# Kernel tuning notes

Hardware: AMD Instinct MI355X
Metric: run time of the kernel (lower is better)

The kernel has to match this reference:

```python
import jax, jax.numpy as jnp
import numpy as np

N, B, D = 100000, 1024, 768  # total nodes, num graphs, feature dim
DE = 64                      # placeholder edge-feat dim (unused, passed through)


def setup_inputs() -> dict:
    key = jax.random.key(0)
    ks = jax.random.split(key, 6)
    feat = jax.random.normal(ks[0], (N, D), jnp.float32)
    vn_feat = jax.random.normal(ks[1], (B, D), jnp.float32)
    edge_feat = jax.random.normal(ks[2], (B, DE), jnp.float32)
    batch = jnp.sort(jax.random.randint(ks[3], (N,), 0, B)).astype(jnp.int32)
    fc_W = jax.random.normal(ks[4], (D, D), jnp.float32) * 0.02
    fc_b = jnp.zeros((D,), jnp.float32)
    proj_W = jax.random.normal(ks[5], (D, D), jnp.float32) * 0.02
    proj_b = jnp.zeros((D,), jnp.float32)
    return dict(feat=feat, vn_feat=vn_feat, edge_feat=edge_feat, batch=batch,
                num_graphs=B, fc_W=fc_W, fc_b=fc_b, proj_W=proj_W, proj_b=proj_b)


def _logsum_pool(feat, batch, num_graphs):
    # r_i = (log N_i / N_i) * sum_k x_k  == mean_pool * log(num_nodes)
    seg_sum = jax.ops.segment_sum(feat, batch, num_segments=num_graphs)  # [B, D]
    cnt = jax.ops.segment_sum(jnp.ones((feat.shape[0],), feat.dtype), batch,
                              num_segments=num_graphs)                   # [B]
    cnt = jnp.maximum(cnt, 1.0)  # guard empty graphs (torch would NaN)
    return (seg_sum / cnt[:, None]) * jnp.log(cnt)[:, None]


def reference(feat, vn_feat, edge_feat, batch, num_graphs, fc_W, fc_b, proj_W, proj_b):
    # 1) scatter-pool node features per graph (logsum pooling)
    pool = _logsum_pool(feat, batch, num_graphs)            # [B, D]
    # 2) FCLayer: Linear -> (norm=none) -> relu -> (dropout=0)
    h = jax.nn.relu((pool + vn_feat) @ fc_W + fc_b)         # [B, D]
    # 3) residual virtual-node update
    vn_new = vn_feat + h                                    # [B, D]
    # 4) project and broadcast-add back to every node
    feat_out = feat + (vn_new @ proj_W + proj_b)[batch]     # [N, D]
    # use_edges=False: edge features pass through unchanged
    return feat_out, vn_new, edge_feat
```

## Files before the change

### kernel.cpp

```cpp
#include <hip/hip_runtime.h>
#include <cmath>

#define THREADS 256
#define PCOLS 192

typedef __attribute__((ext_vector_type(8))) short bf16x8;
typedef __attribute__((ext_vector_type(4))) float f32x4;

__device__ __forceinline__ short f2bf(float f) {
    return (short)(__builtin_bit_cast(unsigned, f) >> 16);
}

typedef const __attribute__((address_space(1))) unsigned int* gas1_t;
typedef __attribute__((address_space(3))) unsigned int* las3_t;
__device__ __forceinline__ void gload16(const short* g, short* l) {
    __builtin_amdgcn_global_load_lds((gas1_t)g, (las3_t)l, 16, 0, 0);
}

__device__ __forceinline__ int lower_bound_i(const int* __restrict__ arr, int n, int val) {
    int lo = 0, hi = n;
    while (lo < hi) {
        int mid = (lo + hi) >> 1;
        if (arr[mid] < val) lo = mid + 1; else hi = mid;
    }
    return lo;
}

__device__ __forceinline__ float4 f4add(float4 a, float4 b) {
    a.x += b.x; a.y += b.y; a.z += b.z; a.w += b.w; return a;
}
__device__ __forceinline__ float4 f4fma(float4 a, float s, float4 b) {
    b.x += a.x * s; b.y += a.y * s; b.z += a.z * s; b.w += a.w * s; return b;
}

__global__ void transpose_bf16(const float* __restrict__ src0, short* __restrict__ dst0,
                               const float* __restrict__ src1, short* __restrict__ dst1,
                               int n) {
    const float* src = blockIdx.z ? src1 : src0;
    short* dst = blockIdx.z ? dst1 : dst0;
    __shared__ short tile[32][33];
    int bx = blockIdx.x * 32, by = blockIdx.y * 32;
    int tx = threadIdx.x, ty = threadIdx.y;
    #pragma unroll
    for (int i = 0; i < 32; i += 8)
        tile[ty + i][tx] = f2bf(src[(size_t)(by + ty + i) * n + bx + tx]);
    __syncthreads();
    #pragma unroll
    for (int i = 0; i < 32; i += 8)
        dst[(size_t)(bx + ty + i) * n + by + tx] = tile[tx][ty + i];
}

__global__ void pool_kernel(const float4* __restrict__ feat4, const float4* __restrict__ vn4,
                            const int* __restrict__ batch, short* __restrict__ xbf,
                            int N, int D4) {
    int g = blockIdx.x;
    __shared__ int s_range[2];
    if (threadIdx.x < 2) s_range[threadIdx.x] = lower_bound_i(batch, N, g + (int)threadIdx.x);
    __syncthreads();
    int lo = s_range[0], hi = s_range[1];
    int cnt = hi - lo;
    float scale = (cnt > 0) ? (logf((float)cnt) / (float)cnt) : 0.f;

    int t = threadIdx.x;
    float4 a0 = {0,0,0,0}, a1 = {0,0,0,0}, a2 = {0,0,0,0}, a3 = {0,0,0,0};
    float4 a4 = {0,0,0,0}, a5 = {0,0,0,0}, a6 = {0,0,0,0}, a7 = {0,0,0,0};

    const float4* __restrict__ p = feat4 + (size_t)lo * D4 + t;
    int r = lo;
    for (; r + 8 <= hi; r += 8) {
        float4 v0 = p[0 * (size_t)D4];
        float4 v1 = p[1 * (size_t)D4];
        float4 v2 = p[2 * (size_t)D4];
        float4 v3 = p[3 * (size_t)D4];
        float4 v4 = p[4 * (size_t)D4];
        float4 v5 = p[5 * (size_t)D4];
        float4 v6 = p[6 * (size_t)D4];
        float4 v7 = p[7 * (size_t)D4];
        a0 = f4add(a0, v0); a1 = f4add(a1, v1); a2 = f4add(a2, v2); a3 = f4add(a3, v3);
        a4 = f4add(a4, v4); a5 = f4add(a5, v5); a6 = f4add(a6, v6); a7 = f4add(a7, v7);
        p += 8 * (size_t)D4;
    }
    for (; r < hi; ++r) {
        a0 = f4add(a0, p[0]);
        p += D4;
    }
    float4 s = f4add(f4add(f4add(a0, a1), f4add(a2, a3)), f4add(f4add(a4, a5), f4add(a6, a7)));
    float4 vnv = vn4[(size_t)g * D4 + t];
    float4 x = f4fma(s, scale, vnv);
    short4 o;
    o.x = f2bf(x.x); o.y = f2bf(x.y); o.z = f2bf(x.z); o.w = f2bf(x.w);
    *(short4*)(xbf + ((size_t)g * D4 + t) * 4) = o;
}

template <bool RELU, bool ADD_RES, bool WRITE_BF>
__global__ __launch_bounds__(256) void gemm_bf(const short* __restrict__ A,
        const short* __restrict__ Wt, const float* __restrict__ bias,
        const float* __restrict__ res, float* __restrict__ out,
        short* __restrict__ out_bf, int Nn, int K) {
    __shared__ short lds[2][2][64 * 32];
    const int tid = threadIdx.x;
    const int lane = tid & 63;
    const int wid = tid >> 6;
    const int wr = wid >> 1, wc = wid & 1;
    const int lrow = lane & 15;
    const int kg = lane >> 4;
    const int tileM = blockIdx.y * 64;
    const int tileN = blockIdx.x * 64;
    const int nk = K / 32;

    f32x4 acc[2][2] = {};

    const int srow = tid >> 2;
    const int sci = (tid & 3) ^ (srow & 3);

    #define STG(buf, kt) do {                                                    \
        short* La = lds[buf][0];                                                 \
        short* Lb = lds[buf][1];                                                 \
        gload16(A  + (size_t)(tileM + srow) * K + (kt) * 32 + sci * 8, La + tid * 8); \
        gload16(Wt + (size_t)(tileN + srow) * K + (kt) * 32 + sci * 8, Lb + tid * 8); \
    } while (0)

    STG(0, 0);
    __syncthreads();

    for (int kt = 0; kt < nk; ++kt) {
        if (kt + 1 < nk) STG((kt + 1) & 1, kt + 1);
        const short* La = lds[kt & 1][0];
        const short* Lb = lds[kt & 1][1];
        bf16x8 a[2], b[2];
        #pragma unroll
        for (int m = 0; m < 2; ++m) {
            int row = wr * 32 + m * 16 + lrow;
            a[m] = *(const bf16x8*)(La + row * 32 + ((kg ^ (row & 3)) * 8));
        }
        #pragma unroll
        for (int n = 0; n < 2; ++n) {
            int col = wc * 32 + n * 16 + lrow;
            b[n] = *(const bf16x8*)(Lb + col * 32 + ((kg ^ (col & 3)) * 8));
        }
        #pragma unroll
        for (int m = 0; m < 2; ++m)
            #pragma unroll
            for (int n = 0; n < 2; ++n)
                acc[m][n] = __builtin_amdgcn_mfma_f32_16x16x32_bf16(a[m], b[n], acc[m][n], 0, 0, 0);
        __syncthreads();
    }

    #pragma unroll
    for (int m = 0; m < 2; ++m) {
        #pragma unroll
        for (int n = 0; n < 2; ++n) {
            int col = tileN + wc * 32 + n * 16 + lrow;
            float bv = bias[col];
            #pragma unroll
            for (int r = 0; r < 4; ++r) {
                int row = tileM + wr * 32 + m * 16 + kg * 4 + r;
                float v = acc[m][n][r] + bv;
                if (RELU) v = fmaxf(v, 0.f);
                if (ADD_RES) v += res[(size_t)row * Nn + col];
                out[(size_t)row * Nn + col] = v;
                if (WRITE_BF) out_bf[(size_t)row * Nn + col] = f2bf(v);
            }
        }
    }
    #undef STG
}

__global__ void node_add_kernel(const float4* __restrict__ feat4, const float4* __restrict__ y4,
                                const int* __restrict__ batch, float* __restrict__ out,
                                int N, int D4) {
    int node = N - 1 - (int)(blockIdx.x * blockDim.y + threadIdx.y);
    if (node < 0) return;
    int t = threadIdx.x;
    int b = batch[node];
    float4 f = feat4[(size_t)node * D4 + t];
    float4 v = y4[(size_t)b * D4 + t];
    f32x4 r;
    r.x = f.x + v.x; r.y = f.y + v.y; r.z = f.z + v.z; r.w = f.w + v.w;
    f32x4* dst = (f32x4*)(out + ((size_t)node * D4 + t) * 4);
    __builtin_nontemporal_store(r, dst);
}

extern "C" void kernel_launch(void* const* d_in, const int* in_sizes, int n_in,
                              void* d_out, int out_size, void* d_ws, size_t ws_size,
                              hipStream_t stream) {
    const float* feat  = (const float*)d_in[0];
    const float* vn    = (const float*)d_in[1];
    const float* edge  = (const float*)d_in[2];
    const int*   batch = (const int*)d_in[3];
    const float* fcW   = (const float*)d_in[5];
    const float* fcb   = (const float*)d_in[6];
    const float* pW    = (const float*)d_in[7];
    const float* pb    = (const float*)d_in[8];

    const int D = in_sizes[6];
    const int N = in_sizes[0] / D;
    const int B = in_sizes[1] / D;
    const int edge_elems = in_sizes[2];
    const int D4 = D / 4;

    float* out_feat = (float*)d_out;
    float* out_vn   = out_feat + (size_t)N * D;
    float* out_edge = out_vn + (size_t)B * D;

    char* ws = (char*)d_ws;
    short* xbf  = (short*)ws;
    short* x2bf = (short*)(ws + (size_t)B * D * 2);
    short* fcWt = (short*)(ws + (size_t)B * D * 4);
    short* pWt  = (short*)(ws + (size_t)B * D * 4 + (size_t)D * D * 2);
    float* y    = (float*)(ws + (size_t)B * D * 4 + (size_t)D * D * 4);

    dim3 tb(32, 8);
    dim3 tg(D / 32, D / 32, 2);
    transpose_bf16<<<tg, tb, 0, stream>>>(fcW, fcWt, pW, pWt, D);

    pool_kernel<<<B, PCOLS, 0, stream>>>((const float4*)feat, (const float4*)vn,
                                         batch, xbf, N, D4);

    dim3 gdim(D / 64, B / 64);
    gemm_bf<true, true, true><<<gdim, THREADS, 0, stream>>>(xbf, fcWt, fcb, vn,
                                                            out_vn, x2bf, D, D);

    gemm_bf<false, false, false><<<gdim, THREADS, 0, stream>>>(x2bf, pWt, pb, nullptr,
                                                               y, nullptr, D, D);

    dim3 nblk(192, 2);
    node_add_kernel<<<(N + 1) / 2, nblk, 0, stream>>>((const float4*)feat, (const float4*)y,
                                                      batch, out_feat, N, D4);

    hipMemcpyAsync(out_edge, edge, (size_t)edge_elems * sizeof(float),
                   hipMemcpyDeviceToDevice, stream);
}
```

Baseline: 188.3 us.

## Partition feat reads into cache-resident prefix and nontemporal suffix across pool and node-add

The pool kernel now reads nodes below a fixed threshold (72000 rows) with normal loads and the rest with nontemporal loads, so roughly the first 220 MB of feat is meant to stay in the large last-level cache. The node-add kernel now walks nodes in forward order and uses normal loads for the cached prefix and nontemporal loads for the suffix, aiming to hit the cached rows on the second pass over feat. The threshold is hardcoded to the cache capacity and input size, so it may thrash or under-use the cache on other configurations. Reversing the traversal order changes the reuse pattern compared with the old reverse-order scheme.

```diff
diff --git a/kernel.cpp b/kernel.cpp
--- a/kernel.cpp
+++ b/kernel.cpp
@@ -3,6 +3,7 @@
 
 #define THREADS 256
 #define PCOLS 192
+#define T_RESIDENT 72000
 
 typedef __attribute__((ext_vector_type(8))) short bf16x8;
 typedef __attribute__((ext_vector_type(4))) float f32x4;
@@ -31,6 +32,16 @@
 }
 __device__ __forceinline__ float4 f4fma(float4 a, float s, float4 b) {
     b.x += a.x * s; b.y += a.y * s; b.z += a.z * s; b.w += a.w * s; return b;
+}
+
+template <bool NT>
+__device__ __forceinline__ float4 ldf4(const float4* p) {
+    if constexpr (NT) {
+        f32x4 v = __builtin_nontemporal_load((const f32x4*)p);
+        float4 r; r.x = v.x; r.y = v.y; r.z = v.z; r.w = v.w; return r;
+    } else {
+        return *p;
+    }
 }
 
 __global__ void transpose_bf16(const float* __restrict__ src0, short* __restrict__ dst0,
@@ -50,9 +61,34 @@
         dst[(size_t)(bx + ty + i) * n + by + tx] = tile[tx][ty + i];
 }
 
+template <bool NT>
+__device__ __forceinline__ void accum8(const float4* __restrict__ base, int a, int b, int D4, int t,
+                                       float4& a0, float4& a1, float4& a2, float4& a3,
+                                       float4& a4, float4& a5, float4& a6, float4& a7) {
+    const float4* __restrict__ p = base + (size_t)a * D4 + t;
+    int r = a;
+    for (; r + 8 <= b; r += 8) {
+        float4 v0 = ldf4<NT>(p + 0 * (size_t)D4);
+        float4 v1 = ldf4<NT>(p + 1 * (size_t)D4);
+        float4 v2 = ldf4<NT>(p + 2 * (size_t)D4);
+        float4 v3 = ldf4<NT>(p + 3 * (size_t)D4);
+        float4 v4 = ldf4<NT>(p + 4 * (size_t)D4);
+        float4 v5 = ldf4<NT>(p + 5 * (size_t)D4);
+        float4 v6 = ldf4<NT>(p + 6 * (size_t)D4);
+        float4 v7 = ldf4<NT>(p + 7 * (size_t)D4);
+        a0 = f4add(a0, v0); a1 = f4add(a1, v1); a2 = f4add(a2, v2); a3 = f4add(a3, v3);
+        a4 = f4add(a4, v4); a5 = f4add(a5, v5); a6 = f4add(a6, v6); a7 = f4add(a7, v7);
+        p += 8 * (size_t)D4;
+    }
+    for (; r < b; ++r) {
+        a0 = f4add(a0, ldf4<NT>(p));
+        p += D4;
+    }
+}
+
 __global__ void pool_kernel(const float4* __restrict__ feat4, const float4* __restrict__ vn4,
                             const int* __restrict__ batch, short* __restrict__ xbf,
-                            int N, int D4) {
+                            int N, int D4, int Tres) {
     int g = blockIdx.x;
     __shared__ int s_range[2];
     if (threadIdx.x < 2) s_range[threadIdx.x] = lower_bound_i(batch, N, g + (int)threadIdx.x);
@@ -65,25 +101,10 @@
     float4 a0 = {0,0,0,0}, a1 = {0,0,0,0}, a2 = {0,0,0,0}, a3 = {0,0,0,0};
     float4 a4 = {0,0,0,0}, a5 = {0,0,0,0}, a6 = {0,0,0,0}, a7 = {0,0,0,0};
 
-    const float4* __restrict__ p = feat4 + (size_t)lo * D4 + t;
-    int r = lo;
-    for (; r + 8 <= hi; r += 8) {
-        float4 v0 = p[0 * (size_t)D4];
-        float4 v1 = p[1 * (size_t)D4];
-        float4 v2 = p[2 * (size_t)D4];
-        float4 v3 = p[3 * (size_t)D4];
-        float4 v4 = p[4 * (size_t)D4];
-        float4 v5 = p[5 * (size_t)D4];
-        float4 v6 = p[6 * (size_t)D4];
-        float4 v7 = p[7 * (size_t)D4];
-        a0 = f4add(a0, v0); a1 = f4add(a1, v1); a2 = f4add(a2, v2); a3 = f4add(a3, v3);
-        a4 = f4add(a4, v4); a5 = f4add(a5, v5); a6 = f4add(a6, v6); a7 = f4add(a7, v7);
-        p += 8 * (size_t)D4;
-    }
-    for (; r < hi; ++r) {
-        a0 = f4add(a0, p[0]);
-        p += D4;
-    }
+    int m = hi < Tres ? hi : (lo > Tres ? lo : Tres);
+    accum8<false>(feat4, lo, m, D4, t, a0, a1, a2, a3, a4, a5, a6, a7);
+    accum8<true >(feat4, m, hi, D4, t, a0, a1, a2, a3, a4, a5, a6, a7);
+
     float4 s = f4add(f4add(f4add(a0, a1), f4add(a2, a3)), f4add(f4add(a4, a5), f4add(a6, a7)));
     float4 vnv = vn4[(size_t)g * D4 + t];
     float4 x = f4fma(s, scale, vnv);
@@ -168,16 +189,17 @@
 
 __global__ void node_add_kernel(const float4* __restrict__ feat4, const float4* __restrict__ y4,
                                 const int* __restrict__ batch, float* __restrict__ out,
-                                int N, int D4) {
-    int node = N - 1 - (int)(blockIdx.x * blockDim.y + threadIdx.y);
-    if (node < 0) return;
+                                int N, int D4, int Tres) {
+    int node = (int)(blockIdx.x * blockDim.y + threadIdx.y);
+    if (node >= N) return;
     int t = threadIdx.x;
     int b = batch[node];
-    float4 f = feat4[(size_t)node * D4 + t];
+    size_t idx = (size_t)node * D4 + t;
+    float4 f = (node < Tres) ? feat4[idx] : ldf4<true>(&feat4[idx]);
     float4 v = y4[(size_t)b * D4 + t];
     f32x4 r;
     r.x = f.x + v.x; r.y = f.y + v.y; r.z = f.z + v.z; r.w = f.w + v.w;
-    f32x4* dst = (f32x4*)(out + ((size_t)node * D4 + t) * 4);
+    f32x4* dst = (f32x4*)(out + idx * 4);
     __builtin_nontemporal_store(r, dst);
 }
 
@@ -215,7 +237,7 @@
     transpose_bf16<<<tg, tb, 0, stream>>>(fcW, fcWt, pW, pWt, D);
 
     pool_kernel<<<B, PCOLS, 0, stream>>>((const float4*)feat, (const float4*)vn,
-                                         batch, xbf, N, D4);
+                                         batch, xbf, N, D4, T_RESIDENT);
 
     dim3 gdim(D / 64, B / 64);
     gemm_bf<true, true, true><<<gdim, THREADS, 0, stream>>>(xbf, fcWt, fcb, vn,
@@ -226,7 +248,7 @@
 
     dim3 nblk(192, 2);
     node_add_kernel<<<(N + 1) / 2, nblk, 0, stream>>>((const float4*)feat, (const float4*)y,
-                                                      batch, out_feat, N, D4);
+                                                      batch, out_feat, N, D4, T_RESIDENT);
 
     hipMemcpyAsync(out_edge, edge, (size_t)edge_elems * sizeof(float),
                    hipMemcpyDeviceToDevice, stream);
```

Result: faster. 182.9 us (-2.9%).

## Stage a bf16 copy of node features in pooling and read it in node add

Applied to the files above, without the earlier changes.

The pooling kernel now also writes a round-to-nearest bf16 copy of every node feature row into workspace, using nontemporal loads. When the workspace is large enough, a new node_add_bf kernel reads that bf16 copy instead of the fp32 features and adds the projected virtual-node row. The goal is to halve the feature bytes read in the final broadcast-add. In exchange, pooling now writes an extra half-size copy, so total memory traffic is roughly unchanged. The passthrough feature values also lose precision in the output, and the reversed node order that reused pooling's recently read rows from cache is dropped.

```diff
diff --git a/kernel.cpp b/kernel.cpp
--- a/kernel.cpp
+++ b/kernel.cpp
@@ -9,6 +9,15 @@
 
 __device__ __forceinline__ short f2bf(float f) {
     return (short)(__builtin_bit_cast(unsigned, f) >> 16);
+}
+__device__ __forceinline__ short f2bf_rne(float f) {
+    unsigned u = __builtin_bit_cast(unsigned, f);
+    unsigned r = (u + 0x7fffu + ((u >> 16) & 1u)) >> 16;
+    return (short)r;
+}
+__device__ __forceinline__ float bf2f(short s) {
+    unsigned u = ((unsigned)(unsigned short)s) << 16;
+    return __builtin_bit_cast(float, u);
 }
 
 typedef const __attribute__((address_space(1))) unsigned int* gas1_t;
@@ -31,6 +40,10 @@
 }
 __device__ __forceinline__ float4 f4fma(float4 a, float s, float4 b) {
     b.x += a.x * s; b.y += a.y * s; b.z += a.z * s; b.w += a.w * s; return b;
+}
+__device__ __forceinline__ float4 ldnt4(const float4* p) {
+    f32x4 v = __builtin_nontemporal_load((const f32x4*)p);
+    float4 r; r.x = v.x; r.y = v.y; r.z = v.z; r.w = v.w; return r;
 }
 
 __global__ void transpose_bf16(const float* __restrict__ src0, short* __restrict__ dst0,
@@ -50,9 +63,10 @@
         dst[(size_t)(bx + ty + i) * n + by + tx] = tile[tx][ty + i];
 }
 
+template <bool SBF>
 __global__ void pool_kernel(const float4* __restrict__ feat4, const float4* __restrict__ vn4,
                             const int* __restrict__ batch, short* __restrict__ xbf,
-                            int N, int D4) {
+                            short* __restrict__ featbf, int N, int D4) {
     int g = blockIdx.x;
     __shared__ int s_range[2];
     if (threadIdx.x < 2) s_range[threadIdx.x] = lower_bound_i(batch, N, g + (int)threadIdx.x);
@@ -66,23 +80,44 @@
     float4 a4 = {0,0,0,0}, a5 = {0,0,0,0}, a6 = {0,0,0,0}, a7 = {0,0,0,0};
 
     const float4* __restrict__ p = feat4 + (size_t)lo * D4 + t;
+    short* __restrict__ pb = featbf + ((size_t)lo * D4 + t) * 4;
+    const size_t rowb = (size_t)D4 * 4;
     int r = lo;
     for (; r + 8 <= hi; r += 8) {
-        float4 v0 = p[0 * (size_t)D4];
-        float4 v1 = p[1 * (size_t)D4];
-        float4 v2 = p[2 * (size_t)D4];
-        float4 v3 = p[3 * (size_t)D4];
-        float4 v4 = p[4 * (size_t)D4];
-        float4 v5 = p[5 * (size_t)D4];
-        float4 v6 = p[6 * (size_t)D4];
-        float4 v7 = p[7 * (size_t)D4];
+        float4 v0 = ldnt4(p + 0 * (size_t)D4);
+        float4 v1 = ldnt4(p + 1 * (size_t)D4);
+        float4 v2 = ldnt4(p + 2 * (size_t)D4);
+        float4 v3 = ldnt4(p + 3 * (size_t)D4);
+        float4 v4 = ldnt4(p + 4 * (size_t)D4);
+        float4 v5 = ldnt4(p + 5 * (size_t)D4);
+        float4 v6 = ldnt4(p + 6 * (size_t)D4);
+        float4 v7 = ldnt4(p + 7 * (size_t)D4);
+        if (SBF) {
+            float4 vv[8] = {v0, v1, v2, v3, v4, v5, v6, v7};
+            #pragma unroll
+            for (int k = 0; k < 8; ++k) {
+                short4 o;
+                o.x = f2bf_rne(vv[k].x); o.y = f2bf_rne(vv[k].y);
+                o.z = f2bf_rne(vv[k].z); o.w = f2bf_rne(vv[k].w);
+                *(short4*)(pb + (size_t)k * rowb) = o;
+            }
+        }
         a0 = f4add(a0, v0); a1 = f4add(a1, v1); a2 = f4add(a2, v2); a3 = f4add(a3, v3);
         a4 = f4add(a4, v4); a5 = f4add(a5, v5); a6 = f4add(a6, v6); a7 = f4add(a7, v7);
         p += 8 * (size_t)D4;
+        pb += 8 * rowb;
     }
     for (; r < hi; ++r) {
-        a0 = f4add(a0, p[0]);
+        float4 v = ldnt4(p);
+        if (SBF) {
+            short4 o;
+            o.x = f2bf_rne(v.x); o.y = f2bf_rne(v.y);
+            o.z = f2bf_rne(v.z); o.w = f2bf_rne(v.w);
+            *(short4*)pb = o;
+        }
+        a0 = f4add(a0, v);
         p += D4;
+        pb += rowb;
     }
     float4 s = f4add(f4add(f4add(a0, a1), f4add(a2, a3)), f4add(f4add(a4, a5), f4add(a6, a7)));
     float4 vnv = vn4[(size_t)g * D4 + t];
@@ -166,19 +201,39 @@
     #undef STG
 }
 
+__global__ void node_add_bf(const short* __restrict__ featbf, const float* __restrict__ y,
+                            const int* __restrict__ batch, float* __restrict__ out, int N) {
+    int node = blockIdx.x * blockDim.y + threadIdx.y;
+    if (node >= N) return;
+    int t = threadIdx.x;
+    int b = batch[node];
+    bf16x8 f = *(const bf16x8*)(featbf + (size_t)node * 768 + t * 8);
+    const float* yp = y + (size_t)b * 768 + t * 8;
+    float4 ya = *(const float4*)yp;
+    float4 yb = *(const float4*)(yp + 4);
+    f32x4 r0, r1;
+    r0.x = bf2f(f[0]) + ya.x; r0.y = bf2f(f[1]) + ya.y;
+    r0.z = bf2f(f[2]) + ya.z; r0.w = bf2f(f[3]) + ya.w;
+    r1.x = bf2f(f[4]) + yb.x; r1.y = bf2f(f[5]) + yb.y;
+    r1.z = bf2f(f[6]) + yb.z; r1.w = bf2f(f[7]) + yb.w;
+    float* op = out + (size_t)node * 768 + t * 8;
+    __builtin_nontemporal_store(r0, (f32x4*)op);
+    __builtin_nontemporal_store(r1, (f32x4*)(op + 4));
+}
+
 __global__ void node_add_kernel(const float4* __restrict__ feat4, const float4* __restrict__ y4,
                                 const int* __restrict__ batch, float* __restrict__ out,
                                 int N, int D4) {
-    int node = N - 1 - (int)(blockIdx.x * blockDim.y + threadIdx.y);
-    if (node < 0) return;
+    int node = (int)(blockIdx.x * blockDim.y + threadIdx.y);
+    if (node >= N) return;
     int t = threadIdx.x;
     int b = batch[node];
-    float4 f = feat4[(size_t)node * D4 + t];
+    size_t idx = (size_t)node * D4 + t;
+    float4 f = feat4[idx];
     float4 v = y4[(size_t)b * D4 + t];
     f32x4 r;
     r.x = f.x + v.x; r.y = f.y + v.y; r.z = f.z + v.z; r.w = f.w + v.w;
-    f32x4* dst = (f32x4*)(out + ((size_t)node * D4 + t) * 4);
-    __builtin_nontemporal_store(r, dst);
+    __builtin_nontemporal_store(r, (f32x4*)(out + idx * 4));
 }
 
 extern "C" void kernel_launch(void* const* d_in, const int* in_sizes, int n_in,
@@ -204,18 +259,25 @@
     float* out_edge = out_vn + (size_t)B * D;
 
     char* ws = (char*)d_ws;
-    short* xbf  = (short*)ws;
-    short* x2bf = (short*)(ws + (size_t)B * D * 2);
-    short* fcWt = (short*)(ws + (size_t)B * D * 4);
-    short* pWt  = (short*)(ws + (size_t)B * D * 4 + (size_t)D * D * 2);
-    float* y    = (float*)(ws + (size_t)B * D * 4 + (size_t)D * D * 4);
+    size_t off = 0;
+    short* xbf  = (short*)(ws + off); off += (size_t)B * D * 2;
+    short* x2bf = (short*)(ws + off); off += (size_t)B * D * 2;
+    short* fcWt = (short*)(ws + off); off += (size_t)D * D * 2;
+    short* pWt  = (short*)(ws + off); off += (size_t)D * D * 2;
+    float* y    = (float*)(ws + off); off += (size_t)B * D * 4;
+    short* featbf = (short*)(ws + off);
+    const bool use_bf = (ws_size >= off + (size_t)N * D * 2);
 
     dim3 tb(32, 8);
     dim3 tg(D / 32, D / 32, 2);
     transpose_bf16<<<tg, tb, 0, stream>>>(fcW, fcWt, pW, pWt, D);
 
-    pool_kernel<<<B, PCOLS, 0, stream>>>((const float4*)feat, (const float4*)vn,
-                                         batch, xbf, N, D4);
+    if (use_bf)
+        pool_kernel<true><<<B, PCOLS, 0, stream>>>((const float4*)feat, (const float4*)vn,
+                                                   batch, xbf, featbf, N, D4);
+    else
+        pool_kernel<false><<<B, PCOLS, 0, stream>>>((const float4*)feat, (const float4*)vn,
+                                                    batch, xbf, nullptr, N, D4);
 
     dim3 gdim(D / 64, B / 64);
     gemm_bf<true, true, true><<<gdim, THREADS, 0, stream>>>(xbf, fcWt, fcb, vn,
@@ -224,9 +286,14 @@
     gemm_bf<false, false, false><<<gdim, THREADS, 0, stream>>>(x2bf, pWt, pb, nullptr,
                                                                y, nullptr, D, D);
 
-    dim3 nblk(192, 2);
-    node_add_kernel<<<(N + 1) / 2, nblk, 0, stream>>>((const float4*)feat, (const float4*)y,
-                                                      batch, out_feat, N, D4);
+    if (use_bf) {
+        dim3 nblk(96, 8);
+        node_add_bf<<<(N + 7) / 8, nblk, 0, stream>>>(featbf, y, batch, out_feat, N);
+    } else {
+        dim3 nblk(192, 2);
+        node_add_kernel<<<(N + 1) / 2, nblk, 0, stream>>>((const float4*)feat, (const float4*)y,
+                                                          batch, out_feat, N, D4);
+    }
 
     hipMemcpyAsync(out_edge, edge, (size_t)edge_elems * sizeof(float),
                    hipMemcpyDeviceToDevice, stream);
```

New measurement: 228.9 us. 1.22x slower.
